# Optimization experiments

Hardware: AMD Instinct MI355X
Metric: run time of the kernel (lower is better)

The kernel has to match this reference:

```python
import jax, jax.numpy as jnp
import numpy as np

N_AGENTS = 5
RNN = 128
ATT = 64
N_ACT = 10
IN_DIM = 256
SIZE = 65535  # multiple of N_AGENTS -> padding branch never taken
TAU = 0.01


def _gru_cell(x, h, w_ih, w_hh, b_ih, b_hh):
    # PyTorch GRUCell math
    gi = x @ w_ih.T + b_ih
    gh = h @ w_hh.T + b_hh
    i_r, i_z, i_n = jnp.split(gi, 3, axis=-1)
    h_r, h_z, h_n = jnp.split(gh, 3, axis=-1)
    r = jax.nn.sigmoid(i_r + h_r)
    z = jax.nn.sigmoid(i_z + h_z)
    n = jnp.tanh(i_n + r * h_n)
    return (1.0 - z) * n + z * h


def _gru_seq(xs, w_ih, w_hh, b_ih, b_hh):
    # xs: [T, B, D]; zero initial hidden, returns all step outputs [T, B, RNN]
    h0 = jnp.zeros((xs.shape[1], RNN), xs.dtype)
    def step(h, x):
        h2 = _gru_cell(x, h, w_ih, w_hh, b_ih, b_hh)
        return h2, h2
    _, ys = jax.lax.scan(step, h0, xs)
    return ys


def setup_inputs():
    key = jax.random.key(0)
    ks = jax.random.split(key, 26)
    def u(k, shape, fan):
        return jax.random.uniform(k, shape, jnp.float32, -1.0, 1.0) / np.sqrt(fan)
    return {
        'obs': jax.random.normal(ks[0], (SIZE, IN_DIM), jnp.float32),
        'hidden_state': jax.random.normal(ks[1], (SIZE, RNN), jnp.float32),
        'enc_w': u(ks[2], (RNN, IN_DIM), IN_DIM), 'enc_b': u(ks[3], (RNN,), IN_DIM),
        'gru_w_ih': u(ks[4], (3 * RNN, RNN), RNN), 'gru_w_hh': u(ks[5], (3 * RNN, RNN), RNN),
        'gru_b_ih': u(ks[6], (3 * RNN,), RNN), 'gru_b_hh': u(ks[7], (3 * RNN,), RNN),
        'bi_w_ih_f': u(ks[8], (3 * RNN, 2 * RNN), RNN), 'bi_w_hh_f': u(ks[9], (3 * RNN, RNN), RNN),
        'bi_b_ih_f': u(ks[10], (3 * RNN,), RNN), 'bi_b_hh_f': u(ks[11], (3 * RNN,), RNN),
        'bi_w_ih_r': u(ks[12], (3 * RNN, 2 * RNN), RNN), 'bi_w_hh_r': u(ks[13], (3 * RNN, RNN), RNN),
        'bi_b_ih_r': u(ks[14], (3 * RNN,), RNN), 'bi_b_hh_r': u(ks[15], (3 * RNN,), RNN),
        'hard_w': u(ks[16], (2, 2 * RNN), 2 * RNN), 'hard_b': u(ks[17], (2,), 2 * RNN),
        'q_w': u(ks[18], (ATT, RNN), RNN),
        'k_w': u(ks[19], (ATT, RNN), RNN),
        'v_w': u(ks[20], (ATT, RNN), RNN), 'v_b': u(ks[21], (ATT,), RNN),
        'dec_w': u(ks[22], (N_ACT, RNN + ATT), RNN + ATT), 'dec_b': u(ks[23], (N_ACT,), RNN + ATT),
    }


def reference(obs, hidden_state, enc_w, enc_b, gru_w_ih, gru_w_hh, gru_b_ih, gru_b_hh,
              bi_w_ih_f, bi_w_hh_f, bi_b_ih_f, bi_b_hh_f,
              bi_w_ih_r, bi_w_hh_r, bi_b_ih_r, bi_b_hh_r,
              hard_w, hard_b, q_w, k_w, v_w, v_b, dec_w, dec_b):
    size = obs.shape[0]
    bpa = size // N_AGENTS  # batch per agent; SIZE is a multiple of N_AGENTS

    x = jax.nn.relu(obs @ enc_w.T + enc_b)
    h_out = _gru_cell(x, hidden_state, gru_w_ih, gru_w_hh, gru_b_ih, gru_b_hh)

    # --- hard attention: pairwise agent features -> bi-GRU -> gumbel-softmax gate ---
    # (computed exactly as in the original; note the original soft_attention
    #  ignores hard_weights, so this does not influence the returned output)
    h = h_out.reshape(bpa, N_AGENTS, RNN)
    nbr = np.array([[j for j in range(N_AGENTS) if j != i] for i in range(N_AGENTS)])  # [n, n-1]
    h_i = jnp.broadcast_to(h[:, :, None, :], (bpa, N_AGENTS, N_AGENTS - 1, RNN))
    h_j = h[:, nbr, :]                              # [bpa, n, n-1, RNN]
    pair = jnp.concatenate([h_i, h_j], axis=-1)     # [bpa, n, n-1, 2*RNN]
    seq = pair.transpose(2, 0, 1, 3).reshape(N_AGENTS - 1, bpa * N_AGENTS, 2 * RNN)
    fwd = _gru_seq(seq, bi_w_ih_f, bi_w_hh_f, bi_b_ih_f, bi_b_hh_f)
    bwd = _gru_seq(seq[::-1], bi_w_ih_r, bi_w_hh_r, bi_b_ih_r, bi_b_hh_r)[::-1]
    h_hard = jnp.concatenate([fwd, bwd], axis=-1)   # [n-1, B, 2*RNN]
    h_hard = h_hard.transpose(1, 0, 2).reshape(-1, 2 * RNN)
    logits = h_hard @ hard_w.T + hard_b             # [B*(n-1), 2]
    u01 = jax.random.uniform(jax.random.key(42), logits.shape, jnp.float32, 1e-10, 1.0)
    gumbel = -jnp.log(-jnp.log(u01))
    gs = jax.nn.softmax((logits + gumbel) / TAU, axis=-1)
    hard_weights = gs[:, 1].reshape(bpa, N_AGENTS, 1, N_AGENTS - 1).transpose(1, 0, 2, 3)
    _ = hard_weights  # unused downstream, matching the original module

    # --- soft attention: original loops per sample doing a 1x1 matmul+softmax;
    #     vectorized here. softmax over a single element is identically 1. ---
    q = h_out @ q_w.T
    k = h_out @ k_w.T
    v = jax.nn.relu(h_out @ v_w.T + v_b)
    score = jnp.sum(q * k, axis=-1, keepdims=True) / np.sqrt(ATT)  # [B,1]
    soft_w = jax.nn.softmax(score, axis=-1)                         # all ones
    x_att = v * soft_w

    final_input = jnp.concatenate([h_out, x_att], axis=-1)
    output = final_input @ dec_w.T + dec_b
    return output, h_out
```

## Files before the change

### kernel.cpp

```cpp
#include <hip/hip_runtime.h>
#include <stdint.h>

#define SIZE 65535

typedef __bf16 bf16x8 __attribute__((ext_vector_type(8)));
typedef float floatx4 __attribute__((ext_vector_type(4)));

#define WS_ENCW 0
#define WS_WIH  32768
#define WS_WHH  81920
#define WS_VW   131072
#define WS_DECW 139264
#define WS_TOT  141184

__device__ __forceinline__ unsigned short f2bf(float f) {
    union { float f; unsigned int u; } v; v.f = f;
    unsigned int u = v.u;
    return (unsigned short)((u + 0x7fffu + ((u >> 16) & 1u)) >> 16);
}
__device__ __forceinline__ float bf2f(unsigned short b) {
    union { unsigned int u; float f; } v; v.u = ((unsigned int)b) << 16;
    return v.f;
}
__device__ __forceinline__ float sigmf(float x) {
    x = fminf(fmaxf(x, -30.f), 30.f);
    return 1.f / (1.f + __expf(-x));
}
__device__ __forceinline__ float tanhfast(float x) {
    x = fminf(fmaxf(x, -15.f), 15.f);
    float e = __expf(2.f * x);
    return (e - 1.f) / (e + 1.f);
}

union BF8 { bf16x8 v; unsigned short s[8]; };

__device__ __forceinline__ bf16x8 cvt8g(const float* p) {
    float4 a = *reinterpret_cast<const float4*>(p);
    float4 b = *reinterpret_cast<const float4*>(p + 4);
    BF8 r;
    r.s[0] = f2bf(a.x); r.s[1] = f2bf(a.y); r.s[2] = f2bf(a.z); r.s[3] = f2bf(a.w);
    r.s[4] = f2bf(b.x); r.s[5] = f2bf(b.y); r.s[6] = f2bf(b.z); r.s[7] = f2bf(b.w);
    return r.v;
}
__device__ __forceinline__ bf16x8 ld8(const unsigned short* p) {
    return *reinterpret_cast<const bf16x8*>(p);
}

__global__ __launch_bounds__(256) void cvt_weights(
    const float* __restrict__ enc_w, const float* __restrict__ w_ih,
    const float* __restrict__ w_hh, const float* __restrict__ v_w,
    const float* __restrict__ dec_w, unsigned short* __restrict__ ws) {
    int i = blockIdx.x * 256 + threadIdx.x;
    if (i >= WS_TOT) return;
    const float* src; int off;
    if (i < WS_WIH)       { src = enc_w; off = WS_ENCW; }
    else if (i < WS_WHH)  { src = w_ih;  off = WS_WIH; }
    else if (i < WS_VW)   { src = w_hh;  off = WS_WHH; }
    else if (i < WS_DECW) { src = v_w;   off = WS_VW; }
    else                  { src = dec_w; off = WS_DECW; }
    ws[i] = f2bf(src[i - off]);
}

__global__ __launch_bounds__(256, 2) void attn_critic_kernel(
    const float* __restrict__ obs,
    const float* __restrict__ hid,
    const float* __restrict__ enc_b,
    const float* __restrict__ b_ih,
    const float* __restrict__ b_hh,
    const float* __restrict__ v_b,
    const float* __restrict__ dec_b,
    const unsigned short* __restrict__ wsw,
    float* __restrict__ out)
{
    __shared__ __align__(16) unsigned short sB[4][32][192];

    const unsigned short* encw = wsw + WS_ENCW;
    const unsigned short* wih  = wsw + WS_WIH;
    const unsigned short* whh  = wsw + WS_WHH;
    const unsigned short* vw   = wsw + WS_VW;
    const unsigned short* decw = wsw + WS_DECW;

    const int tid  = threadIdx.x;
    const int wave = tid >> 6;
    const int lane = tid & 63;
    const int l15  = lane & 15;
    const int quad = lane >> 4;
    const int wrow0 = (blockIdx.x * 4 + wave) * 32;
    unsigned short (*S)[192] = sB[wave];

    int rA0 = wrow0 + l15;      rA0 = (rA0 < SIZE) ? rA0 : (SIZE - 1);
    int rA1 = wrow0 + 16 + l15; rA1 = (rA1 < SIZE) ? rA1 : (SIZE - 1);

    bf16x8 aob[2][8];
    {
        const float* o0 = obs + (size_t)rA0 * 256;
        const float* o1 = obs + (size_t)rA1 * 256;
#pragma unroll
        for (int kt = 0; kt < 8; ++kt) {
            aob[0][kt] = cvt8g(o0 + kt * 32 + quad * 8);
            aob[1][kt] = cvt8g(o1 + kt * 32 + quad * 8);
        }
    }

    floatx4 acc1[2][8];
#pragma unroll
    for (int nt = 0; nt < 8; ++nt) {
        acc1[0][nt] = floatx4{0.f, 0.f, 0.f, 0.f};
        acc1[1][nt] = floatx4{0.f, 0.f, 0.f, 0.f};
    }
#pragma unroll 1
    for (int kt = 0; kt < 8; ++kt) {
#pragma unroll
        for (int nt = 0; nt < 8; ++nt) {
            bf16x8 b = ld8(encw + (nt * 16 + l15) * 256 + kt * 32 + quad * 8);
            acc1[0][nt] = __builtin_amdgcn_mfma_f32_16x16x32_bf16(aob[0][kt], b, acc1[0][nt], 0, 0, 0);
            acc1[1][nt] = __builtin_amdgcn_mfma_f32_16x16x32_bf16(aob[1][kt], b, acc1[1][nt], 0, 0, 0);
        }
    }

    bf16x8 hf[2][4];
    {
        const float* h0 = hid + (size_t)rA0 * 128;
        const float* h1 = hid + (size_t)rA1 * 128;
#pragma unroll
        for (int kt = 0; kt < 4; ++kt) {
            hf[0][kt] = cvt8g(h0 + kt * 32 + quad * 8);
            hf[1][kt] = cvt8g(h1 + kt * 32 + quad * 8);
        }
    }

#pragma unroll
    for (int nt = 0; nt < 8; ++nt) {
        float bias = enc_b[nt * 16 + l15];
#pragma unroll
        for (int r = 0; r < 4; ++r) {
            S[quad * 4 + r][nt * 16 + l15]      = f2bf(fmaxf(acc1[0][nt][r] + bias, 0.f));
            S[16 + quad * 4 + r][nt * 16 + l15] = f2bf(fmaxf(acc1[1][nt][r] + bias, 0.f));
        }
    }
    bf16x8 xf[2][4];
#pragma unroll
    for (int kt = 0; kt < 4; ++kt) {
        xf[0][kt] = ld8(&S[l15][kt * 32 + quad * 8]);
        xf[1][kt] = ld8(&S[16 + l15][kt * 32 + quad * 8]);
    }

    float* out_h = out + (size_t)SIZE * 10;

#pragma unroll 1
    for (int nt = 0; nt < 8; ++nt) {
        const int nr = nt * 16 + l15;
        floatx4 gir[2], giz[2], gin[2], ghr[2], ghz[2], ghn[2];
#pragma unroll
        for (int m = 0; m < 2; ++m) {
            gir[m] = floatx4{0.f,0.f,0.f,0.f}; giz[m] = gir[m]; gin[m] = gir[m];
            ghr[m] = gir[m]; ghz[m] = gir[m]; ghn[m] = gir[m];
        }
#pragma unroll
        for (int kt = 0; kt < 4; ++kt) {
            const int ko = kt * 32 + quad * 8;
            bf16x8 bir = ld8(wih + (size_t)(nr)       * 128 + ko);
            bf16x8 biz = ld8(wih + (size_t)(nr + 128) * 128 + ko);
            bf16x8 bin = ld8(wih + (size_t)(nr + 256) * 128 + ko);
            bf16x8 bhr = ld8(whh + (size_t)(nr)       * 128 + ko);
            bf16x8 bhz = ld8(whh + (size_t)(nr + 128) * 128 + ko);
            bf16x8 bhn = ld8(whh + (size_t)(nr + 256) * 128 + ko);
#pragma unroll
            for (int m = 0; m < 2; ++m) {
                gir[m] = __builtin_amdgcn_mfma_f32_16x16x32_bf16(xf[m][kt], bir, gir[m], 0, 0, 0);
                giz[m] = __builtin_amdgcn_mfma_f32_16x16x32_bf16(xf[m][kt], biz, giz[m], 0, 0, 0);
                gin[m] = __builtin_amdgcn_mfma_f32_16x16x32_bf16(xf[m][kt], bin, gin[m], 0, 0, 0);
                ghr[m] = __builtin_amdgcn_mfma_f32_16x16x32_bf16(hf[m][kt], bhr, ghr[m], 0, 0, 0);
                ghz[m] = __builtin_amdgcn_mfma_f32_16x16x32_bf16(hf[m][kt], bhz, ghz[m], 0, 0, 0);
                ghn[m] = __builtin_amdgcn_mfma_f32_16x16x32_bf16(hf[m][kt], bhn, ghn[m], 0, 0, 0);
            }
        }
        const float bir_ = b_ih[nr], biz_ = b_ih[nr + 128], bin_ = b_ih[nr + 256];
        const float bhr_ = b_hh[nr], bhz_ = b_hh[nr + 128], bhn_ = b_hh[nr + 256];
#pragma unroll
        for (int m = 0; m < 2; ++m) {
#pragma unroll
            for (int r = 0; r < 4; ++r) {
                const int grow = wrow0 + m * 16 + quad * 4 + r;
                const int rowc = (grow < SIZE) ? grow : (SIZE - 1);
                float hprev = hid[(size_t)rowc * 128 + nr];
                float rg = sigmf(gir[m][r] + bir_ + ghr[m][r] + bhr_);
                float zg = sigmf(giz[m][r] + biz_ + ghz[m][r] + bhz_);
                float ng = tanhfast(gin[m][r] + bin_ + rg * (ghn[m][r] + bhn_));
                float ho = (1.f - zg) * ng + zg * hprev;
                S[m * 16 + quad * 4 + r][nr] = f2bf(ho);
                if (grow < SIZE) out_h[(size_t)grow * 128 + nr] = ho;
            }
        }
    }

    bf16x8 af[2][4];
#pragma unroll
    for (int kt = 0; kt < 4; ++kt) {
        af[0][kt] = ld8(&S[l15][kt * 32 + quad * 8]);
        af[1][kt] = ld8(&S[16 + l15][kt * 32 + quad * 8]);
    }
#pragma unroll 1
    for (int nt = 0; nt < 4; ++nt) {
        floatx4 a3[2];
        a3[0] = floatx4{0.f, 0.f, 0.f, 0.f}; a3[1] = a3[0];
#pragma unroll
        for (int kt = 0; kt < 4; ++kt) {
            bf16x8 b = ld8(vw + (nt * 16 + l15) * 128 + kt * 32 + quad * 8);
            a3[0] = __builtin_amdgcn_mfma_f32_16x16x32_bf16(af[0][kt], b, a3[0], 0, 0, 0);
            a3[1] = __builtin_amdgcn_mfma_f32_16x16x32_bf16(af[1][kt], b, a3[1], 0, 0, 0);
        }
        float bias = v_b[nt * 16 + l15];
#pragma unroll
        for (int m = 0; m < 2; ++m)
#pragma unroll
            for (int r = 0; r < 4; ++r)
                S[m * 16 + quad * 4 + r][128 + nt * 16 + l15] =
                    f2bf(fmaxf(a3[m][r] + bias, 0.f));
    }

    {
        floatx4 a4[2];
        a4[0] = floatx4{0.f, 0.f, 0.f, 0.f}; a4[1] = a4[0];
        const int wr = (l15 < 10) ? l15 : 9;
#pragma unroll
        for (int kt = 0; kt < 6; ++kt) {
            bf16x8 b  = ld8(decw + wr * 192 + kt * 32 + quad * 8);
            bf16x8 a0 = ld8(&S[l15][kt * 32 + quad * 8]);
            bf16x8 a1 = ld8(&S[16 + l15][kt * 32 + quad * 8]);
            a4[0] = __builtin_amdgcn_mfma_f32_16x16x32_bf16(a0, b, a4[0], 0, 0, 0);
            a4[1] = __builtin_amdgcn_mfma_f32_16x16x32_bf16(a1, b, a4[1], 0, 0, 0);
        }
        if (l15 < 10) {
            float bias = dec_b[l15];
#pragma unroll
            for (int m = 0; m < 2; ++m)
#pragma unroll
                for (int r = 0; r < 4; ++r) {
                    int grow = wrow0 + m * 16 + quad * 4 + r;
                    if (grow < SIZE) out[(size_t)grow * 10 + l15] = a4[m][r] + bias;
                }
        }
    }
}

extern "C" void kernel_launch(void* const* d_in, const int* in_sizes, int n_in,
                              void* d_out, int out_size, void* d_ws, size_t ws_size,
                              hipStream_t stream) {
    const float* obs   = (const float*)d_in[0];
    const float* hid   = (const float*)d_in[1];
    const float* enc_w = (const float*)d_in[2];
    const float* enc_b = (const float*)d_in[3];
    const float* w_ih  = (const float*)d_in[4];
    const float* w_hh  = (const float*)d_in[5];
    const float* b_ih  = (const float*)d_in[6];
    const float* b_hh  = (const float*)d_in[7];
    const float* v_w   = (const float*)d_in[20];
    const float* v_b   = (const float*)d_in[21];
    const float* dec_w = (const float*)d_in[22];
    const float* dec_b = (const float*)d_in[23];
    unsigned short* wsw = (unsigned short*)d_ws;
    float* out = (float*)d_out;

    hipLaunchKernelGGL(cvt_weights, dim3((WS_TOT + 255) / 256), dim3(256), 0, stream,
                       enc_w, w_ih, w_hh, v_w, dec_w, wsw);
    hipLaunchKernelGGL(attn_critic_kernel, dim3(512), dim3(256), 0, stream,
                       obs, hid, enc_b, b_ih, b_hh, v_b, dec_b, wsw, out);
}
```

Baseline: 256.0 us.

## Pre-swizzle weights into MFMA fragment order and coalesce output stores via LDS

The conversion kernel now writes the bf16 weights in per-lane MFMA fragment order, so each wave loads every B fragment as one contiguous 512-byte block instead of strided row reads. The encoder loop is reordered to keep two accumulators per column tile rather than sixteen, which lowers register pressure. The h_out and action outputs are staged in shared memory and written row-contiguously, replacing scattered per-element stores. One side effect is that h_out is now written from the bf16-rounded LDS copy rather than the fp32 value, which lowers output precision.

```diff
diff --git a/kernel.cpp b/kernel.cpp
--- a/kernel.cpp
+++ b/kernel.cpp
@@ -11,7 +11,7 @@
 #define WS_WHH  81920
 #define WS_VW   131072
 #define WS_DECW 139264
-#define WS_TOT  141184
+#define WS_TOTC 17792
 
 __device__ __forceinline__ unsigned short f2bf(float f) {
     union { float f; unsigned int u; } v; v.f = f;
@@ -50,15 +50,41 @@
     const float* __restrict__ enc_w, const float* __restrict__ w_ih,
     const float* __restrict__ w_hh, const float* __restrict__ v_w,
     const float* __restrict__ dec_w, unsigned short* __restrict__ ws) {
-    int i = blockIdx.x * 256 + threadIdx.x;
-    if (i >= WS_TOT) return;
-    const float* src; int off;
-    if (i < WS_WIH)       { src = enc_w; off = WS_ENCW; }
-    else if (i < WS_WHH)  { src = w_ih;  off = WS_WIH; }
-    else if (i < WS_VW)   { src = w_hh;  off = WS_WHH; }
-    else if (i < WS_DECW) { src = v_w;   off = WS_VW; }
-    else                  { src = dec_w; off = WS_DECW; }
-    ws[i] = f2bf(src[i - off]);
+    int c = blockIdx.x * 256 + threadIdx.x;
+    if (c >= WS_TOTC) return;
+    const int lane = c & 63;
+    const int l = lane & 15;
+    const int q = lane >> 4;
+    const float* src; int row, col, stride; bool zero = false;
+    if (c < 4096) {
+        int lt = c >> 6; int nt = lt >> 3, kt = lt & 7;
+        row = nt * 16 + l; col = kt * 32 + q * 8; src = enc_w; stride = 256;
+    } else if (c < 10240) {
+        int lt = (c - 4096) >> 6; int nt = lt / 12; int r2 = lt % 12;
+        int g = r2 >> 2, kt = r2 & 3;
+        row = g * 128 + nt * 16 + l; col = kt * 32 + q * 8; src = w_ih; stride = 128;
+    } else if (c < 16384) {
+        int lt = (c - 10240) >> 6; int nt = lt / 12; int r2 = lt % 12;
+        int g = r2 >> 2, kt = r2 & 3;
+        row = g * 128 + nt * 16 + l; col = kt * 32 + q * 8; src = w_hh; stride = 128;
+    } else if (c < 17408) {
+        int lt = (c - 16384) >> 6; int nt = lt >> 2, kt = lt & 3;
+        row = nt * 16 + l; col = kt * 32 + q * 8; src = v_w; stride = 128;
+    } else {
+        int kt = (c - 17408) >> 6;
+        row = l; col = kt * 32 + q * 8; src = dec_w; stride = 192;
+        zero = (l >= 10);
+    }
+    float4 a, b;
+    if (zero) { a = make_float4(0.f,0.f,0.f,0.f); b = a; }
+    else {
+        const float* p = src + (size_t)row * stride + col;
+        a = *reinterpret_cast<const float4*>(p);
+        b = *reinterpret_cast<const float4*>(p + 4);
+    }
+    unsigned short* d = ws + (size_t)c * 8;
+    d[0]=f2bf(a.x); d[1]=f2bf(a.y); d[2]=f2bf(a.z); d[3]=f2bf(a.w);
+    d[4]=f2bf(b.x); d[5]=f2bf(b.y); d[6]=f2bf(b.z); d[7]=f2bf(b.w);
 }
 
 __global__ __launch_bounds__(256, 2) void attn_critic_kernel(
@@ -72,13 +98,9 @@
     const unsigned short* __restrict__ wsw,
     float* __restrict__ out)
 {
-    __shared__ __align__(16) unsigned short sB[4][32][192];
-
-    const unsigned short* encw = wsw + WS_ENCW;
-    const unsigned short* wih  = wsw + WS_WIH;
-    const unsigned short* whh  = wsw + WS_WHH;
-    const unsigned short* vw   = wsw + WS_VW;
-    const unsigned short* decw = wsw + WS_DECW;
+    __shared__ __align__(16) unsigned short sA[4][32][136];
+    __shared__ __align__(16) unsigned short sV[4][32][72];
+    __shared__ __align__(16) float sO[4][32][10];
 
     const int tid  = threadIdx.x;
     const int wave = tid >> 6;
@@ -86,12 +108,11 @@
     const int l15  = lane & 15;
     const int quad = lane >> 4;
     const int wrow0 = (blockIdx.x * 4 + wave) * 32;
-    unsigned short (*S)[192] = sB[wave];
 
     int rA0 = wrow0 + l15;      rA0 = (rA0 < SIZE) ? rA0 : (SIZE - 1);
     int rA1 = wrow0 + 16 + l15; rA1 = (rA1 < SIZE) ? rA1 : (SIZE - 1);
 
-    bf16x8 aob[2][8];
+    bf16x8 aob[2][8], hf[2][4];
     {
         const float* o0 = obs + (size_t)rA0 * 256;
         const float* o1 = obs + (size_t)rA1 * 256;
@@ -100,26 +121,6 @@
             aob[0][kt] = cvt8g(o0 + kt * 32 + quad * 8);
             aob[1][kt] = cvt8g(o1 + kt * 32 + quad * 8);
         }
-    }
-
-    floatx4 acc1[2][8];
-#pragma unroll
-    for (int nt = 0; nt < 8; ++nt) {
-        acc1[0][nt] = floatx4{0.f, 0.f, 0.f, 0.f};
-        acc1[1][nt] = floatx4{0.f, 0.f, 0.f, 0.f};
-    }
-#pragma unroll 1
-    for (int kt = 0; kt < 8; ++kt) {
-#pragma unroll
-        for (int nt = 0; nt < 8; ++nt) {
-            bf16x8 b = ld8(encw + (nt * 16 + l15) * 256 + kt * 32 + quad * 8);
-            acc1[0][nt] = __builtin_amdgcn_mfma_f32_16x16x32_bf16(aob[0][kt], b, acc1[0][nt], 0, 0, 0);
-            acc1[1][nt] = __builtin_amdgcn_mfma_f32_16x16x32_bf16(aob[1][kt], b, acc1[1][nt], 0, 0, 0);
-        }
-    }
-
-    bf16x8 hf[2][4];
-    {
         const float* h0 = hid + (size_t)rA0 * 128;
         const float* h1 = hid + (size_t)rA1 * 128;
 #pragma unroll
@@ -128,118 +129,144 @@
             hf[1][kt] = cvt8g(h1 + kt * 32 + quad * 8);
         }
     }
-
-#pragma unroll
-    for (int nt = 0; nt < 8; ++nt) {
-        float bias = enc_b[nt * 16 + l15];
-#pragma unroll
-        for (int r = 0; r < 4; ++r) {
-            S[quad * 4 + r][nt * 16 + l15]      = f2bf(fmaxf(acc1[0][nt][r] + bias, 0.f));
-            S[16 + quad * 4 + r][nt * 16 + l15] = f2bf(fmaxf(acc1[1][nt][r] + bias, 0.f));
+    __builtin_amdgcn_sched_barrier(0);
+
+    {
+        const unsigned short* encf = wsw + WS_ENCW + lane * 8;
+#pragma unroll 2
+        for (int nt = 0; nt < 8; ++nt) {
+            floatx4 a0 = floatx4{0.f,0.f,0.f,0.f}, a1 = a0;
+#pragma unroll
+            for (int kt = 0; kt < 8; ++kt) {
+                bf16x8 b = ld8(encf + (size_t)(nt * 8 + kt) * 512);
+                a0 = __builtin_amdgcn_mfma_f32_16x16x32_bf16(aob[0][kt], b, a0, 0, 0, 0);
+                a1 = __builtin_amdgcn_mfma_f32_16x16x32_bf16(aob[1][kt], b, a1, 0, 0, 0);
+            }
+            float bias = enc_b[nt * 16 + l15];
+#pragma unroll
+            for (int r = 0; r < 4; ++r) {
+                sA[wave][quad * 4 + r][nt * 16 + l15]      = f2bf(fmaxf(a0[r] + bias, 0.f));
+                sA[wave][16 + quad * 4 + r][nt * 16 + l15] = f2bf(fmaxf(a1[r] + bias, 0.f));
+            }
         }
     }
     bf16x8 xf[2][4];
 #pragma unroll
     for (int kt = 0; kt < 4; ++kt) {
-        xf[0][kt] = ld8(&S[l15][kt * 32 + quad * 8]);
-        xf[1][kt] = ld8(&S[16 + l15][kt * 32 + quad * 8]);
-    }
-
-    float* out_h = out + (size_t)SIZE * 10;
-
+        xf[0][kt] = ld8(&sA[wave][l15][kt * 32 + quad * 8]);
+        xf[1][kt] = ld8(&sA[wave][16 + l15][kt * 32 + quad * 8]);
+    }
+
+    {
+        const unsigned short* wihf = wsw + WS_WIH + lane * 8;
+        const unsigned short* whhf = wsw + WS_WHH + lane * 8;
 #pragma unroll 1
-    for (int nt = 0; nt < 8; ++nt) {
-        const int nr = nt * 16 + l15;
-        floatx4 gir[2], giz[2], gin[2], ghr[2], ghz[2], ghn[2];
-#pragma unroll
-        for (int m = 0; m < 2; ++m) {
-            gir[m] = floatx4{0.f,0.f,0.f,0.f}; giz[m] = gir[m]; gin[m] = gir[m];
-            ghr[m] = gir[m]; ghz[m] = gir[m]; ghn[m] = gir[m];
-        }
-#pragma unroll
-        for (int kt = 0; kt < 4; ++kt) {
-            const int ko = kt * 32 + quad * 8;
-            bf16x8 bir = ld8(wih + (size_t)(nr)       * 128 + ko);
-            bf16x8 biz = ld8(wih + (size_t)(nr + 128) * 128 + ko);
-            bf16x8 bin = ld8(wih + (size_t)(nr + 256) * 128 + ko);
-            bf16x8 bhr = ld8(whh + (size_t)(nr)       * 128 + ko);
-            bf16x8 bhz = ld8(whh + (size_t)(nr + 128) * 128 + ko);
-            bf16x8 bhn = ld8(whh + (size_t)(nr + 256) * 128 + ko);
-#pragma unroll
-            for (int m = 0; m < 2; ++m) {
-                gir[m] = __builtin_amdgcn_mfma_f32_16x16x32_bf16(xf[m][kt], bir, gir[m], 0, 0, 0);
-                giz[m] = __builtin_amdgcn_mfma_f32_16x16x32_bf16(xf[m][kt], biz, giz[m], 0, 0, 0);
-                gin[m] = __builtin_amdgcn_mfma_f32_16x16x32_bf16(xf[m][kt], bin, gin[m], 0, 0, 0);
-                ghr[m] = __builtin_amdgcn_mfma_f32_16x16x32_bf16(hf[m][kt], bhr, ghr[m], 0, 0, 0);
-                ghz[m] = __builtin_amdgcn_mfma_f32_16x16x32_bf16(hf[m][kt], bhz, ghz[m], 0, 0, 0);
-                ghn[m] = __builtin_amdgcn_mfma_f32_16x16x32_bf16(hf[m][kt], bhn, ghn[m], 0, 0, 0);
-            }
-        }
-        const float bir_ = b_ih[nr], biz_ = b_ih[nr + 128], bin_ = b_ih[nr + 256];
-        const float bhr_ = b_hh[nr], bhz_ = b_hh[nr + 128], bhn_ = b_hh[nr + 256];
-#pragma unroll
-        for (int m = 0; m < 2; ++m) {
+        for (int nt = 0; nt < 8; ++nt) {
+            const int nr = nt * 16 + l15;
+            floatx4 gi[3][2], gh[3][2];
+#pragma unroll
+            for (int g = 0; g < 3; ++g) {
+                gi[g][0] = floatx4{0.f,0.f,0.f,0.f}; gi[g][1] = gi[g][0];
+                gh[g][0] = gi[g][0]; gh[g][1] = gi[g][0];
+            }
+#pragma unroll
+            for (int g = 0; g < 3; ++g)
+#pragma unroll
+                for (int kt = 0; kt < 4; ++kt) {
+                    bf16x8 bi = ld8(wihf + (size_t)((nt * 3 + g) * 4 + kt) * 512);
+                    bf16x8 bh = ld8(whhf + (size_t)((nt * 3 + g) * 4 + kt) * 512);
+                    gi[g][0] = __builtin_amdgcn_mfma_f32_16x16x32_bf16(xf[0][kt], bi, gi[g][0], 0, 0, 0);
+                    gi[g][1] = __builtin_amdgcn_mfma_f32_16x16x32_bf16(xf[1][kt], bi, gi[g][1], 0, 0, 0);
+                    gh[g][0] = __builtin_amdgcn_mfma_f32_16x16x32_bf16(hf[0][kt], bh, gh[g][0], 0, 0, 0);
+                    gh[g][1] = __builtin_amdgcn_mfma_f32_16x16x32_bf16(hf[1][kt], bh, gh[g][1], 0, 0, 0);
+                }
+            const float bir_ = b_ih[nr], biz_ = b_ih[nr + 128], bin_ = b_ih[nr + 256];
+            const float bhr_ = b_hh[nr], bhz_ = b_hh[nr + 128], bhn_ = b_hh[nr + 256];
+#pragma unroll
+            for (int m = 0; m < 2; ++m)
+#pragma unroll
+                for (int r = 0; r < 4; ++r) {
+                    const int grow = wrow0 + m * 16 + quad * 4 + r;
+                    const int rowc = (grow < SIZE) ? grow : (SIZE - 1);
+                    float hprev = hid[(size_t)rowc * 128 + nr];
+                    float rg = sigmf(gi[0][m][r] + bir_ + gh[0][m][r] + bhr_);
+                    float zg = sigmf(gi[1][m][r] + biz_ + gh[1][m][r] + bhz_);
+                    float ng = tanhfast(gi[2][m][r] + bin_ + rg * (gh[2][m][r] + bhn_));
+                    float ho = (1.f - zg) * ng + zg * hprev;
+                    sA[wave][m * 16 + quad * 4 + r][nr] = f2bf(ho);
+                }
+        }
+    }
+
+    {
+        float* out_h = out + (size_t)SIZE * 10;
+#pragma unroll 1
+        for (int it = 0; it < 16; ++it) {
+            int idx = it * 256 + lane * 4;
+            int rr = idx >> 7, cc = idx & 127;
+            int grow = wrow0 + rr;
+            if (grow < SIZE) {
+                float2 p0 = make_float2(bf2f(sA[wave][rr][cc]),     bf2f(sA[wave][rr][cc + 1]));
+                float2 p1 = make_float2(bf2f(sA[wave][rr][cc + 2]), bf2f(sA[wave][rr][cc + 3]));
+                float* dst = out_h + (size_t)grow * 128 + cc;
+                *reinterpret_cast<float2*>(dst)     = p0;
+                *reinterpret_cast<float2*>(dst + 2) = p1;
+            }
+        }
+    }
+
+    bf16x8 af[2][4];
+#pragma unroll
+    for (int kt = 0; kt < 4; ++kt) {
+        af[0][kt] = ld8(&sA[wave][l15][kt * 32 + quad * 8]);
+        af[1][kt] = ld8(&sA[wave][16 + l15][kt * 32 + quad * 8]);
+    }
+    {
+        const unsigned short* vwf = wsw + WS_VW + lane * 8;
+#pragma unroll 1
+        for (int nt = 0; nt < 4; ++nt) {
+            floatx4 a0 = floatx4{0.f,0.f,0.f,0.f}, a1 = a0;
+#pragma unroll
+            for (int kt = 0; kt < 4; ++kt) {
+                bf16x8 b = ld8(vwf + (size_t)(nt * 4 + kt) * 512);
+                a0 = __builtin_amdgcn_mfma_f32_16x16x32_bf16(af[0][kt], b, a0, 0, 0, 0);
+                a1 = __builtin_amdgcn_mfma_f32_16x16x32_bf16(af[1][kt], b, a1, 0, 0, 0);
+            }
+            float bias = v_b[nt * 16 + l15];
 #pragma unroll
             for (int r = 0; r < 4; ++r) {
-                const int grow = wrow0 + m * 16 + quad * 4 + r;
-                const int rowc = (grow < SIZE) ? grow : (SIZE - 1);
-                float hprev = hid[(size_t)rowc * 128 + nr];
-                float rg = sigmf(gir[m][r] + bir_ + ghr[m][r] + bhr_);
-                float zg = sigmf(giz[m][r] + biz_ + ghz[m][r] + bhz_);
-                float ng = tanhfast(gin[m][r] + bin_ + rg * (ghn[m][r] + bhn_));
-                float ho = (1.f - zg) * ng + zg * hprev;
-                S[m * 16 + quad * 4 + r][nr] = f2bf(ho);
-                if (grow < SIZE) out_h[(size_t)grow * 128 + nr] = ho;
-            }
-        }
-    }
-
-    bf16x8 af[2][4];
-#pragma unroll
-    for (int kt = 0; kt < 4; ++kt) {
-        af[0][kt] = ld8(&S[l15][kt * 32 + quad * 8]);
-        af[1][kt] = ld8(&S[16 + l15][kt * 32 + quad * 8]);
-    }
-#pragma unroll 1
-    for (int nt = 0; nt < 4; ++nt) {
-        floatx4 a3[2];
-        a3[0] = floatx4{0.f, 0.f, 0.f, 0.f}; a3[1] = a3[0];
-#pragma unroll
-        for (int kt = 0; kt < 4; ++kt) {
-            bf16x8 b = ld8(vw + (nt * 16 + l15) * 128 + kt * 32 + quad * 8);
-            a3[0] = __builtin_amdgcn_mfma_f32_16x16x32_bf16(af[0][kt], b, a3[0], 0, 0, 0);
-            a3[1] = __builtin_amdgcn_mfma_f32_16x16x32_bf16(af[1][kt], b, a3[1], 0, 0, 0);
-        }
-        float bias = v_b[nt * 16 + l15];
-#pragma unroll
-        for (int m = 0; m < 2; ++m)
-#pragma unroll
-            for (int r = 0; r < 4; ++r)
-                S[m * 16 + quad * 4 + r][128 + nt * 16 + l15] =
-                    f2bf(fmaxf(a3[m][r] + bias, 0.f));
-    }
-
-    {
-        floatx4 a4[2];
-        a4[0] = floatx4{0.f, 0.f, 0.f, 0.f}; a4[1] = a4[0];
-        const int wr = (l15 < 10) ? l15 : 9;
+                sV[wave][quad * 4 + r][nt * 16 + l15]      = f2bf(fmaxf(a0[r] + bias, 0.f));
+                sV[wave][16 + quad * 4 + r][nt * 16 + l15] = f2bf(fmaxf(a1[r] + bias, 0.f));
+            }
+        }
+    }
+
+    {
+        const unsigned short* decf = wsw + WS_DECW + lane * 8;
+        floatx4 d0 = floatx4{0.f,0.f,0.f,0.f}, d1 = d0;
 #pragma unroll
         for (int kt = 0; kt < 6; ++kt) {
-            bf16x8 b  = ld8(decw + wr * 192 + kt * 32 + quad * 8);
-            bf16x8 a0 = ld8(&S[l15][kt * 32 + quad * 8]);
-            bf16x8 a1 = ld8(&S[16 + l15][kt * 32 + quad * 8]);
-            a4[0] = __builtin_amdgcn_mfma_f32_16x16x32_bf16(a0, b, a4[0], 0, 0, 0);
-            a4[1] = __builtin_amdgcn_mfma_f32_16x16x32_bf16(a1, b, a4[1], 0, 0, 0);
+            bf16x8 b = ld8(decf + (size_t)kt * 512);
+            bf16x8 a0 = (kt < 4) ? af[0][kt] : ld8(&sV[wave][l15][(kt - 4) * 32 + quad * 8]);
+            bf16x8 a1 = (kt < 4) ? af[1][kt] : ld8(&sV[wave][16 + l15][(kt - 4) * 32 + quad * 8]);
+            d0 = __builtin_amdgcn_mfma_f32_16x16x32_bf16(a0, b, d0, 0, 0, 0);
+            d1 = __builtin_amdgcn_mfma_f32_16x16x32_bf16(a1, b, d1, 0, 0, 0);
         }
         if (l15 < 10) {
             float bias = dec_b[l15];
 #pragma unroll
-            for (int m = 0; m < 2; ++m)
-#pragma unroll
-                for (int r = 0; r < 4; ++r) {
-                    int grow = wrow0 + m * 16 + quad * 4 + r;
-                    if (grow < SIZE) out[(size_t)grow * 10 + l15] = a4[m][r] + bias;
-                }
+            for (int r = 0; r < 4; ++r) {
+                sO[wave][quad * 4 + r][l15]      = d0[r] + bias;
+                sO[wave][16 + quad * 4 + r][l15] = d1[r] + bias;
+            }
+        }
+#pragma unroll
+        for (int j = 0; j < 5; ++j) {
+            int idx = j * 64 + lane;
+            int row = idx / 10, col = idx % 10;
+            int grow = wrow0 + row;
+            if (grow < SIZE)
+                out[(size_t)grow * 10 + col] = sO[wave][row][col];
         }
     }
 }
@@ -262,7 +289,7 @@
     unsigned short* wsw = (unsigned short*)d_ws;
     float* out = (float*)d_out;
 
-    hipLaunchKernelGGL(cvt_weights, dim3((WS_TOT + 255) / 256), dim3(256), 0, stream,
+    hipLaunchKernelGGL(cvt_weights, dim3((WS_TOTC + 255) / 256), dim3(256), 0, stream,
                        enc_w, w_ih, w_hh, v_w, dec_w, wsw);
     hipLaunchKernelGGL(attn_critic_kernel, dim3(512), dim3(256), 0, stream,
                        obs, hid, enc_b, b_ih, b_hh, v_b, dec_b, wsw, out);
```

Result: faster. 221.2 us (-13.6%).
